# Kernel optimization log

Hardware: AMD Instinct MI355X
Metric: run time of the kernel (lower is better)

Reference implementation:

```python
import jax, jax.numpy as jnp
import numpy as np

NUM_EMBEDDINGS = 2048
EMBEDDING_DIM = 128
BETA = 0.25


def setup_inputs() -> dict:
    key = jax.random.key(0)
    k1, k2 = jax.random.split(key)
    z = jax.random.normal(k1, (64, 32, 32, EMBEDDING_DIM), dtype=jnp.float32)
    # nn.Embedding init: uniform(-1/K, 1/K)
    emb = jax.random.uniform(k2, (NUM_EMBEDDINGS, EMBEDDING_DIM), dtype=jnp.float32,
                             minval=-1.0 / NUM_EMBEDDINGS, maxval=1.0 / NUM_EMBEDDINGS)
    return {"z": z, "emb": emb}


def reference(z, emb):
    beta = BETA
    flat = z.reshape(-1, EMBEDDING_DIM)  # [N, D]
    dist = (jnp.sum(flat * flat, axis=1, keepdims=True)
            - 2.0 * flat @ emb.T
            + jnp.sum(emb * emb, axis=1))
    indices = jnp.argmin(dist, axis=1)  # [N]
    quantized = emb[indices].reshape(z.shape)
    # commitment / codebook loss
    loss = (jnp.mean((jax.lax.stop_gradient(quantized) - z) ** 2)
            + beta * jnp.mean((quantized - jax.lax.stop_gradient(z)) ** 2))
    # straight-through estimator
    quantized_st = z + jax.lax.stop_gradient(quantized - z)
    indices_out = indices.reshape(z.shape[0], -1)
    return quantized_st, indices_out, loss
```

## Files before the change

kernel.cpp:

```cpp
#include <hip/hip_runtime.h>

#define NUM_EMB 2048
#define DIM     128
#define NVEC    65536
#define MARGIN  1.0e-3f
#define CAP     32
#define CHUNK   256
#define NCHUNK  (NUM_EMB / CHUNK)
#define ES      136
#define ZS      132

typedef float  f32x4 __attribute__((ext_vector_type(4)));
typedef short  s16x8 __attribute__((ext_vector_type(8)));

__device__ __forceinline__ ushort f2bf(float f) {
    unsigned u = __float_as_uint(f);
    u = (u + 0x7fffu + ((u >> 16) & 1u)) >> 16;
    return (ushort)u;
}

__device__ __forceinline__ float np_pairwise_sumsq_128(const float* __restrict__ p)
{
    float r[8];
    #pragma unroll
    for (int j = 0; j < 8; ++j) { float v = p[j]; r[j] = __fmul_rn(v, v); }
    #pragma unroll
    for (int i = 8; i < 128; i += 8)
        #pragma unroll
        for (int j = 0; j < 8; ++j) { float v = p[i + j]; r[j] = __fadd_rn(r[j], __fmul_rn(v, v)); }
    float s01 = __fadd_rn(r[0], r[1]);
    float s23 = __fadd_rn(r[2], r[3]);
    float s45 = __fadd_rn(r[4], r[5]);
    float s67 = __fadd_rn(r[6], r[7]);
    return __fadd_rn(__fadd_rn(s01, s23), __fadd_rn(s45, s67));
}

__device__ __forceinline__ float dot_seg(const float4* __restrict__ zp,
                                         const float4* __restrict__ ep,
                                         int seg, float dot)
{
    float4 e[8], zz[8];
    #pragma unroll
    for (int i = 0; i < 8; ++i) { e[i] = ep[seg * 8 + i]; zz[i] = zp[seg * 8 + i]; }
    #pragma unroll
    for (int i = 0; i < 8; ++i) {
        dot = fmaf(zz[i].x, e[i].x, dot);
        dot = fmaf(zz[i].y, e[i].y, dot);
        dot = fmaf(zz[i].z, e[i].z, dot);
        dot = fmaf(zz[i].w, e[i].w, dot);
    }
    return dot;
}

__global__ __launch_bounds__(256)
void prep_kernel(const float* __restrict__ emb,
                 float* __restrict__ enorm,
                 float* __restrict__ accum,
                 unsigned* __restrict__ cand_cnt,
                 ushort* __restrict__ emb_bf)
{
    int g = blockIdx.x * 256 + threadIdx.x;
    cand_cnt[g] = 0u;
    if (g == 0) *accum = 0.0f;

    float4 v = ((const float4*)emb)[g];
    ushort4 b;
    b.x = f2bf(v.x); b.y = f2bf(v.y); b.z = f2bf(v.z); b.w = f2bf(v.w);
    ((ushort4*)emb_bf)[g] = b;

    if (g < NUM_EMB)
        enorm[g] = np_pairwise_sumsq_128(emb + (size_t)g * DIM);
}

__global__ __launch_bounds__(1024, 1)
void approx_kernel(const float* __restrict__ z,
                   const ushort* __restrict__ emb_bf,
                   const float* __restrict__ enorm,
                   unsigned* __restrict__ cand_cnt,
                   ushort* __restrict__ cand)
{
    __shared__ __align__(16) ushort eS[CHUNK * ES];
    __shared__ float cS[CHUNK];

    const int tid  = threadIdx.x;
    const int w    = tid >> 6;
    const int lane = tid & 63;
    const int col  = lane & 15;
    const int quad = lane >> 4;
    const int rowbase = blockIdx.x * 256 + w * 16;

    s16x8 afrag[4];
    {
        const float* zr = z + (size_t)(rowbase + col) * DIM;
        #pragma unroll
        for (int kt = 0; kt < 4; ++kt) {
            const float4* p = (const float4*)(zr + kt * 32 + quad * 8);
            float4 f0 = p[0], f1 = p[1];
            s16x8 a;
            a[0] = (short)f2bf(f0.x); a[1] = (short)f2bf(f0.y);
            a[2] = (short)f2bf(f0.z); a[3] = (short)f2bf(f0.w);
            a[4] = (short)f2bf(f1.x); a[5] = (short)f2bf(f1.y);
            a[6] = (short)f2bf(f1.z); a[7] = (short)f2bf(f1.w);
            afrag[kt] = a;
        }
    }

    float minv[4], thr[4];
    #pragma unroll
    for (int r = 0; r < 4; ++r) minv[r] = 3.0e38f;

    for (int vis = 0; vis < 9; ++vis) {
        const int c = (vis == 0) ? 0 : (vis - 1);
        __syncthreads();
        const uint4* src = (const uint4*)(emb_bf + (size_t)c * CHUNK * DIM);
        #pragma unroll
        for (int i = 0; i < 4; ++i) {
            int li   = i * 1024 + tid;
            int code = li >> 4, fc = li & 15;
            *(uint4*)&eS[code * ES + fc * 8] = src[li];
        }
        if (tid < CHUNK) cS[tid] = enorm[c * CHUNK + tid];
        __syncthreads();

        #pragma unroll 4
        for (int t = 0; t < 16; ++t) {
            s16x8 bfrag[4];
            #pragma unroll
            for (int kt = 0; kt < 4; ++kt)
                bfrag[kt] = *(const s16x8*)&eS[(t * 16 + col) * ES + kt * 32 + quad * 8];

            f32x4 a = {0.0f, 0.0f, 0.0f, 0.0f};
            #pragma unroll
            for (int kt = 0; kt < 4; ++kt)
                a = __builtin_amdgcn_mfma_f32_16x16x32_bf16(afrag[kt], bfrag[kt], a, 0, 0, 0);

            float Cc     = cS[t * 16 + col];
            int   code_g = c * CHUNK + t * 16 + col;
            #pragma unroll
            for (int r = 0; r < 4; ++r) {
                float g = fmaf(-2.0f, a[r], Cc);
                minv[r] = fminf(minv[r], g);
                if (vis > 0 && g <= thr[r]) {
                    int row_g = rowbase + quad * 4 + r;
                    unsigned pos = atomicAdd(&cand_cnt[row_g], 1u);
                    if (pos < CAP) cand[(size_t)row_g * CAP + pos] = (ushort)code_g;
                }
            }
        }

        #pragma unroll
        for (int r = 0; r < 4; ++r) {
            float v = minv[r];
            v = fminf(v, __shfl_xor(v, 1, 64));
            v = fminf(v, __shfl_xor(v, 2, 64));
            v = fminf(v, __shfl_xor(v, 4, 64));
            v = fminf(v, __shfl_xor(v, 8, 64));
            minv[r] = v;
            thr[r]  = v + MARGIN;
        }
    }
}

__global__ __launch_bounds__(256)
void rerank_kernel(const float* __restrict__ z,
                   const float* __restrict__ emb,
                   const float* __restrict__ enorm,
                   const unsigned* __restrict__ cand_cnt,
                   const ushort* __restrict__ cand,
                   float* __restrict__ out_q,
                   float* __restrict__ out_idx_f,
                   float* __restrict__ accum)
{
    __shared__ float zs[64 * ZS];
    __shared__ float As[64];
    __shared__ int   bidx[64];
    __shared__ int   ovf_list[64];
    __shared__ int   ovf_n;
    __shared__ float rv[4];
    __shared__ int   rvi[4];
    __shared__ float wsum[4];

    const int tid = threadIdx.x;
    const int m0  = blockIdx.x * 64;
    if (tid == 0) ovf_n = 0;

    #pragma unroll
    for (int i = 0; i < 8; ++i) {
        int li = tid + i * 256;
        int m  = li >> 5, dc = li & 31;
        float4 v = ((const float4*)(z + (size_t)(m0 + m) * DIM))[dc];
        *(float4*)&zs[m * ZS + dc * 4] = v;
    }
    __syncthreads();
    if (tid < 64) As[tid] = np_pairwise_sumsq_128(&zs[tid * ZS]);
    __syncthreads();

    const int row_l = tid >> 2;
    const int sub   = tid & 3;
    const int row_g = m0 + row_l;
    const unsigned cnt = cand_cnt[row_g];
    const float A = As[row_l];
    const float4* zp = (const float4*)&zs[row_l * ZS];

    float bv = 3.0e38f;
    int   bi = 0x7fffffff;

    if (cnt <= CAP) {
        for (unsigned ci = sub; ci < cnt; ci += 4) {
            int j = (int)cand[(size_t)row_g * CAP + ci];
            const float4* ep = (const float4*)(emb + (size_t)j * DIM);
            float dot = 0.0f;
            #pragma unroll
            for (int seg = 0; seg < 4; ++seg) dot = dot_seg(zp, ep, seg, dot);
            float t1 = fmaf(-2.0f, dot, A);
            float s  = __fadd_rn(t1, enorm[j]);
            if (s < bv || (s == bv && j < bi)) { bv = s; bi = j; }
        }
    }
    #pragma unroll
    for (int off = 1; off <= 2; off <<= 1) {
        float v  = __shfl_xor(bv, off, 64);
        int   ix = __shfl_xor(bi, off, 64);
        if (v < bv || (v == bv && ix < bi)) { bv = v; bi = ix; }
    }
    if (sub == 0) {
        if (cnt <= CAP) bidx[row_l] = bi;
        else { int p = atomicAdd(&ovf_n, 1); ovf_list[p] = row_l; }
    }
    __syncthreads();

    const int n_ovf = ovf_n;
    for (int o = 0; o < n_ovf; ++o) {
        const int rl = ovf_list[o];
        const float Ar = As[rl];
        const float4* zp2 = (const float4*)&zs[rl * ZS];
        float bv2 = 3.0e38f;
        int   bi2 = 0x7fffffff;
        for (int jj = 0; jj < 8; ++jj) {
            int j = tid * 8 + jj;
            const float4* ep = (const float4*)(emb + (size_t)j * DIM);
            float dot = 0.0f;
            #pragma unroll
            for (int seg = 0; seg < 4; ++seg) dot = dot_seg(zp2, ep, seg, dot);
            float t1 = fmaf(-2.0f, dot, Ar);
            float s  = __fadd_rn(t1, enorm[j]);
            if (s < bv2) { bv2 = s; bi2 = j; }
        }
        #pragma unroll
        for (int off = 1; off < 64; off <<= 1) {
            float v  = __shfl_xor(bv2, off, 64);
            int   ix = __shfl_xor(bi2, off, 64);
            if (v < bv2 || (v == bv2 && ix < bi2)) { bv2 = v; bi2 = ix; }
        }
        if ((tid & 63) == 0) { rv[tid >> 6] = bv2; rvi[tid >> 6] = bi2; }
        __syncthreads();
        if (tid == 0) {
            float fv = rv[0]; int fi = rvi[0];
            #pragma unroll
            for (int ww = 1; ww < 4; ++ww) {
                if (rv[ww] < fv || (rv[ww] == fv && rvi[ww] < fi)) { fv = rv[ww]; fi = rvi[ww]; }
            }
            bidx[rl] = fi;
        }
        __syncthreads();
    }

    if (tid < 64) out_idx_f[m0 + tid] = (float)bidx[tid];

    float part = 0.0f;
    #pragma unroll
    for (int i = 0; i < 8; ++i) {
        int li = tid + i * 256;
        int m  = li >> 5, dc = li & 31;
        int j  = bidx[m];
        float4 q  = ((const float4*)(emb + (size_t)j * DIM))[dc];
        float4 zv = *(const float4*)&zs[m * ZS + dc * 4];
        float4 o;
        o.x = __fadd_rn(zv.x, __fsub_rn(q.x, zv.x));
        o.y = __fadd_rn(zv.y, __fsub_rn(q.y, zv.y));
        o.z = __fadd_rn(zv.z, __fsub_rn(q.z, zv.z));
        o.w = __fadd_rn(zv.w, __fsub_rn(q.w, zv.w));
        ((float4*)out_q)[(size_t)(m0 + m) * 32 + dc] = o;
        float dx = q.x - zv.x, dy = q.y - zv.y, dz = q.z - zv.z, dw = q.w - zv.w;
        part += dx * dx + dy * dy + dz * dz + dw * dw;
    }
    #pragma unroll
    for (int off = 32; off > 0; off >>= 1)
        part += __shfl_down(part, off, 64);
    if ((tid & 63) == 0) wsum[tid >> 6] = part;
    __syncthreads();
    if (tid == 0) atomicAdd(accum, wsum[0] + wsum[1] + wsum[2] + wsum[3]);
}

__global__ void finalize_kernel(const float* __restrict__ accum,
                                float* __restrict__ out_loss)
{
    *out_loss = 1.25f * (*accum) / 8388608.0f;
}

extern "C" void kernel_launch(void* const* d_in, const int* in_sizes, int n_in,
                              void* d_out, int out_size, void* d_ws, size_t ws_size,
                              hipStream_t stream)
{
    const float* z   = (const float*)d_in[0];
    const float* emb = (const float*)d_in[1];
    float* out = (float*)d_out;

    char*     ws       = (char*)d_ws;
    float*    enorm    = (float*)ws;
    float*    accum    = (float*)(ws + 8192);
    unsigned* cand_cnt = (unsigned*)(ws + 16384);
    ushort*   cand     = (ushort*)(ws + 16384 + 262144);
    ushort*   emb_bf   = (ushort*)(ws + 16384 + 262144 + 4194304);

    prep_kernel   <<<NVEC / 256, 256,  0, stream>>>(emb, enorm, accum, cand_cnt, emb_bf);
    approx_kernel <<<256,        1024, 0, stream>>>(z, emb_bf, enorm, cand_cnt, cand);
    rerank_kernel <<<NVEC / 64,  256,  0, stream>>>(z, emb, enorm, cand_cnt, cand,
                                                    out, out + 8388608, accum);
    finalize_kernel<<<1, 1, 0, stream>>>(accum, out + 8388608 + 65536);
}
```

Before: 226.3 us.

## Pair waves over 32-row tiles splitting codebook chunk halves with shared thresholds

Each wave now computes two 16-row tiles against half of each 256-code chunk, so every B fragment loaded from LDS feeds two MFMAs. Partner waves exchange their running maxima through shared memory to form a common pruning threshold. The distance is folded into the accumulator as x·e - 0.5||e||² by preloading the bias, which removes the per-element fma. This adds shared-memory exchange traffic and more registers, and the partner's maximum lags by one chunk, so candidate filtering is slightly looser.

```diff
diff --git a/kernel.cpp b/kernel.cpp
--- a/kernel.cpp
+++ b/kernel.cpp
@@ -81,17 +81,21 @@
 {
     __shared__ __align__(16) ushort eS[CHUNK * ES];
     __shared__ float cS[CHUNK];
+    __shared__ float vS[16][32];
 
     const int tid  = threadIdx.x;
     const int w    = tid >> 6;
     const int lane = tid & 63;
     const int col  = lane & 15;
     const int quad = lane >> 4;
-    const int rowbase = blockIdx.x * 256 + w * 16;
-
-    s16x8 afrag[4];
-    {
-        const float* zr = z + (size_t)(rowbase + col) * DIM;
+    const int rg   = w >> 1;
+    const int ch   = w & 1;
+    const int rowbase = blockIdx.x * 256 + rg * 32;
+
+    s16x8 afrag[2][4];
+    #pragma unroll
+    for (int rt = 0; rt < 2; ++rt) {
+        const float* zr = z + (size_t)(rowbase + rt * 16 + col) * DIM;
         #pragma unroll
         for (int kt = 0; kt < 4; ++kt) {
             const float4* p = (const float4*)(zr + kt * 32 + quad * 8);
@@ -101,17 +105,30 @@
             a[2] = (short)f2bf(f0.z); a[3] = (short)f2bf(f0.w);
             a[4] = (short)f2bf(f1.x); a[5] = (short)f2bf(f1.y);
             a[6] = (short)f2bf(f1.z); a[7] = (short)f2bf(f1.w);
-            afrag[kt] = a;
-        }
-    }
-
-    float minv[4], thr[4];
-    #pragma unroll
-    for (int r = 0; r < 4; ++r) minv[r] = 3.0e38f;
+            afrag[rt][kt] = a;
+        }
+    }
+
+    const ushort* eH = eS + ch * 128 * ES;
+    const float*  cH = cS + ch * 128;
+
+    float vmax[8], thr[8];
+    #pragma unroll
+    for (int i = 0; i < 8; ++i) { vmax[i] = -3.0e38f; thr[i] = 3.0e38f; }
 
     for (int vis = 0; vis < 9; ++vis) {
         const int c = (vis == 0) ? 0 : (vis - 1);
         __syncthreads();
+
+        if (vis > 0) {
+            #pragma unroll
+            for (int i = 0; i < 8; ++i) {
+                float v = fmaxf(vmax[i], vS[w ^ 1][(i >> 2) * 16 + quad * 4 + (i & 3)]);
+                vmax[i] = v;
+                thr[i]  = v - 0.5f * MARGIN;
+            }
+        }
+
         const uint4* src = (const uint4*)(emb_bf + (size_t)c * CHUNK * DIM);
         #pragma unroll
         for (int i = 0; i < 4; ++i) {
@@ -119,44 +136,59 @@
             int code = li >> 4, fc = li & 15;
             *(uint4*)&eS[code * ES + fc * 8] = src[li];
         }
-        if (tid < CHUNK) cS[tid] = enorm[c * CHUNK + tid];
+        if (tid < CHUNK) cS[tid] = -0.5f * enorm[c * CHUNK + tid];
         __syncthreads();
 
         #pragma unroll 4
-        for (int t = 0; t < 16; ++t) {
+        for (int t = 0; t < 8; ++t) {
             s16x8 bfrag[4];
             #pragma unroll
             for (int kt = 0; kt < 4; ++kt)
-                bfrag[kt] = *(const s16x8*)&eS[(t * 16 + col) * ES + kt * 32 + quad * 8];
-
-            f32x4 a = {0.0f, 0.0f, 0.0f, 0.0f};
-            #pragma unroll
-            for (int kt = 0; kt < 4; ++kt)
-                a = __builtin_amdgcn_mfma_f32_16x16x32_bf16(afrag[kt], bfrag[kt], a, 0, 0, 0);
-
-            float Cc     = cS[t * 16 + col];
-            int   code_g = c * CHUNK + t * 16 + col;
+                bfrag[kt] = *(const s16x8*)&eH[(t * 16 + col) * ES + kt * 32 + quad * 8];
+
+            float h = cH[t * 16 + col];
+            f32x4 a0 = {h, h, h, h};
+            f32x4 a1 = {h, h, h, h};
+            #pragma unroll
+            for (int kt = 0; kt < 4; ++kt) {
+                a0 = __builtin_amdgcn_mfma_f32_16x16x32_bf16(afrag[0][kt], bfrag[kt], a0, 0, 0, 0);
+                a1 = __builtin_amdgcn_mfma_f32_16x16x32_bf16(afrag[1][kt], bfrag[kt], a1, 0, 0, 0);
+            }
+
+            const int code_g = c * CHUNK + ch * 128 + t * 16 + col;
             #pragma unroll
             for (int r = 0; r < 4; ++r) {
-                float g = fmaf(-2.0f, a[r], Cc);
-                minv[r] = fminf(minv[r], g);
-                if (vis > 0 && g <= thr[r]) {
+                float v0 = a0[r];
+                vmax[r] = fmaxf(vmax[r], v0);
+                if (vis > 0 && v0 >= thr[r]) {
                     int row_g = rowbase + quad * 4 + r;
                     unsigned pos = atomicAdd(&cand_cnt[row_g], 1u);
                     if (pos < CAP) cand[(size_t)row_g * CAP + pos] = (ushort)code_g;
                 }
+                float v1 = a1[r];
+                vmax[4 + r] = fmaxf(vmax[4 + r], v1);
+                if (vis > 0 && v1 >= thr[4 + r]) {
+                    int row_g = rowbase + 16 + quad * 4 + r;
+                    unsigned pos = atomicAdd(&cand_cnt[row_g], 1u);
+                    if (pos < CAP) cand[(size_t)row_g * CAP + pos] = (ushort)code_g;
+                }
             }
         }
 
         #pragma unroll
-        for (int r = 0; r < 4; ++r) {
-            float v = minv[r];
-            v = fminf(v, __shfl_xor(v, 1, 64));
-            v = fminf(v, __shfl_xor(v, 2, 64));
-            v = fminf(v, __shfl_xor(v, 4, 64));
-            v = fminf(v, __shfl_xor(v, 8, 64));
-            minv[r] = v;
-            thr[r]  = v + MARGIN;
+        for (int i = 0; i < 8; ++i) {
+            float v = vmax[i];
+            v = fmaxf(v, __shfl_xor(v, 1, 64));
+            v = fmaxf(v, __shfl_xor(v, 2, 64));
+            v = fmaxf(v, __shfl_xor(v, 4, 64));
+            v = fmaxf(v, __shfl_xor(v, 8, 64));
+            vmax[i] = v;
+            thr[i]  = v - 0.5f * MARGIN;
+        }
+        if (col == 0) {
+            #pragma unroll
+            for (int i = 0; i < 8; ++i)
+                vS[w][(i >> 2) * 16 + quad * 4 + (i & 3)] = vmax[i];
         }
     }
 }
```

Result: slower. 232.5 us (+2.7%).

## Split codebook chunk across wave pairs and fold norm into MFMA accumulator

Applied to the files above, without the earlier changes.

The approximate search kernel now has each pair of waves share 16 rows, with each wave scanning half of every 256-code chunk. Running maxima are exchanged through shared memory so both halves use a common pruning threshold. The grid doubles to 512 blocks, so more of the GPU's compute units get work. The codebook norm term is pre-scaled by -0.5 and used as the MFMA accumulator's starting value, which turns the distance into a max-score and drops one FMA per element. Each block still loads the full chunk into shared memory, so per-row staging traffic doubles, and the threshold sharing across the pair lags by one chunk.

```diff
diff --git a/kernel.cpp b/kernel.cpp
--- a/kernel.cpp
+++ b/kernel.cpp
@@ -72,7 +72,7 @@
         enorm[g] = np_pairwise_sumsq_128(emb + (size_t)g * DIM);
 }
 
-__global__ __launch_bounds__(1024, 1)
+__global__ __launch_bounds__(1024, 8)
 void approx_kernel(const float* __restrict__ z,
                    const ushort* __restrict__ emb_bf,
                    const float* __restrict__ enorm,
@@ -81,13 +81,16 @@
 {
     __shared__ __align__(16) ushort eS[CHUNK * ES];
     __shared__ float cS[CHUNK];
+    __shared__ float vS[16][16];
 
     const int tid  = threadIdx.x;
     const int w    = tid >> 6;
     const int lane = tid & 63;
     const int col  = lane & 15;
     const int quad = lane >> 4;
-    const int rowbase = blockIdx.x * 256 + w * 16;
+    const int rg   = w >> 1;
+    const int ch   = w & 1;
+    const int rowbase = blockIdx.x * 128 + rg * 16;
 
     s16x8 afrag[4];
     {
@@ -105,13 +108,26 @@
         }
     }
 
-    float minv[4], thr[4];
-    #pragma unroll
-    for (int r = 0; r < 4; ++r) minv[r] = 3.0e38f;
+    const ushort* eH = eS + ch * 128 * ES;
+    const float*  cH = cS + ch * 128;
+
+    float vmax[4], thr[4];
+    #pragma unroll
+    for (int r = 0; r < 4; ++r) { vmax[r] = -3.0e38f; thr[r] = 3.0e38f; }
 
     for (int vis = 0; vis < 9; ++vis) {
         const int c = (vis == 0) ? 0 : (vis - 1);
         __syncthreads();
+
+        if (vis > 0) {
+            #pragma unroll
+            for (int r = 0; r < 4; ++r) {
+                float v = fmaxf(vmax[r], vS[w ^ 1][quad * 4 + r]);
+                vmax[r] = v;
+                thr[r]  = v - 0.5f * MARGIN;
+            }
+        }
+
         const uint4* src = (const uint4*)(emb_bf + (size_t)c * CHUNK * DIM);
         #pragma unroll
         for (int i = 0; i < 4; ++i) {
@@ -119,28 +135,28 @@
             int code = li >> 4, fc = li & 15;
             *(uint4*)&eS[code * ES + fc * 8] = src[li];
         }
-        if (tid < CHUNK) cS[tid] = enorm[c * CHUNK + tid];
+        if (tid < CHUNK) cS[tid] = -0.5f * enorm[c * CHUNK + tid];
         __syncthreads();
 
         #pragma unroll 4
-        for (int t = 0; t < 16; ++t) {
+        for (int t = 0; t < 8; ++t) {
             s16x8 bfrag[4];
             #pragma unroll
             for (int kt = 0; kt < 4; ++kt)
-                bfrag[kt] = *(const s16x8*)&eS[(t * 16 + col) * ES + kt * 32 + quad * 8];
-
-            f32x4 a = {0.0f, 0.0f, 0.0f, 0.0f};
+                bfrag[kt] = *(const s16x8*)&eH[(t * 16 + col) * ES + kt * 32 + quad * 8];
+
+            float h = cH[t * 16 + col];
+            f32x4 a = {h, h, h, h};
             #pragma unroll
             for (int kt = 0; kt < 4; ++kt)
                 a = __builtin_amdgcn_mfma_f32_16x16x32_bf16(afrag[kt], bfrag[kt], a, 0, 0, 0);
 
-            float Cc     = cS[t * 16 + col];
-            int   code_g = c * CHUNK + t * 16 + col;
+            const int code_g = c * CHUNK + ch * 128 + t * 16 + col;
             #pragma unroll
             for (int r = 0; r < 4; ++r) {
-                float g = fmaf(-2.0f, a[r], Cc);
-                minv[r] = fminf(minv[r], g);
-                if (vis > 0 && g <= thr[r]) {
+                float v = a[r];
+                vmax[r] = fmaxf(vmax[r], v);
+                if (vis > 0 && v >= thr[r]) {
                     int row_g = rowbase + quad * 4 + r;
                     unsigned pos = atomicAdd(&cand_cnt[row_g], 1u);
                     if (pos < CAP) cand[(size_t)row_g * CAP + pos] = (ushort)code_g;
@@ -150,13 +166,18 @@
 
         #pragma unroll
         for (int r = 0; r < 4; ++r) {
-            float v = minv[r];
-            v = fminf(v, __shfl_xor(v, 1, 64));
-            v = fminf(v, __shfl_xor(v, 2, 64));
-            v = fminf(v, __shfl_xor(v, 4, 64));
-            v = fminf(v, __shfl_xor(v, 8, 64));
-            minv[r] = v;
-            thr[r]  = v + MARGIN;
+            float v = vmax[r];
+            v = fmaxf(v, __shfl_xor(v, 1, 64));
+            v = fmaxf(v, __shfl_xor(v, 2, 64));
+            v = fmaxf(v, __shfl_xor(v, 4, 64));
+            v = fmaxf(v, __shfl_xor(v, 8, 64));
+            vmax[r] = v;
+            thr[r]  = v - 0.5f * MARGIN;
+        }
+        if (col == 0) {
+            #pragma unroll
+            for (int r = 0; r < 4; ++r)
+                vS[w][quad * 4 + r] = vmax[r];
         }
     }
 }
@@ -314,7 +335,7 @@
     ushort*   emb_bf   = (ushort*)(ws + 16384 + 262144 + 4194304);
 
     prep_kernel   <<<NVEC / 256, 256,  0, stream>>>(emb, enorm, accum, cand_cnt, emb_bf);
-    approx_kernel <<<256,        1024, 0, stream>>>(z, emb_bf, enorm, cand_cnt, cand);
+    approx_kernel <<<NVEC / 128, 1024, 0, stream>>>(z, emb_bf, enorm, cand_cnt, cand);
     rerank_kernel <<<NVEC / 64,  256,  0, stream>>>(z, emb, enorm, cand_cnt, cand,
                                                     out, out + 8388608, accum);
     finalize_kernel<<<1, 1, 0, stream>>>(accum, out + 8388608 + 65536);
```

Measured after the change: 244.5 us. 8.0% more time.
